# Optimization experiments

Measured on AMD Instinct MI355X. Metric: run time of the kernel, lower is better.

Reference implementation:

```python
import jax, jax.numpy as jnp
import numpy as np

D_MODEL = 768
N_HEADS = 12
D_K = D_MODEL // N_HEADS
LORA_RANK = 8
LORA_ALPHA = 16
SCALING = LORA_ALPHA / LORA_RANK  # lora scaling = alpha / rank
SCALE = float(np.sqrt(D_K))      # attention scale = sqrt(d_k)


def setup_inputs() -> dict:
    key = jax.random.key(0)
    ks = jax.random.split(key, 16)
    s = 0.02
    inp = {
        "x": jax.random.normal(ks[0], (1, 4096, D_MODEL), dtype=jnp.float32),
        # base projections: torch Linear weights are [out, in]
        "wq": jax.random.normal(ks[1], (D_MODEL, D_MODEL), dtype=jnp.float32) * s,
        "bq": jax.random.normal(ks[2], (D_MODEL,), dtype=jnp.float32) * s,
        "wk": jax.random.normal(ks[3], (D_MODEL, D_MODEL), dtype=jnp.float32) * s,
        "bk": jax.random.normal(ks[4], (D_MODEL,), dtype=jnp.float32) * s,
        "wv": jax.random.normal(ks[5], (D_MODEL, D_MODEL), dtype=jnp.float32) * s,
        "bv": jax.random.normal(ks[6], (D_MODEL,), dtype=jnp.float32) * s,
        "wo": jax.random.normal(ks[7], (D_MODEL, D_MODEL), dtype=jnp.float32) * s,
        "bo": jax.random.normal(ks[8], (D_MODEL,), dtype=jnp.float32) * s,
        # LoRA adapters (no bias): down [rank, d_model], up [d_model, rank]
        "wq_down": jax.random.normal(ks[9], (LORA_RANK, D_MODEL), dtype=jnp.float32) * s,
        "wq_up": jax.random.normal(ks[10], (D_MODEL, LORA_RANK), dtype=jnp.float32) * s,
        "wk_down": jax.random.normal(ks[11], (LORA_RANK, D_MODEL), dtype=jnp.float32) * s,
        "wk_up": jax.random.normal(ks[12], (D_MODEL, LORA_RANK), dtype=jnp.float32) * s,
        "wv_down": jax.random.normal(ks[13], (LORA_RANK, D_MODEL), dtype=jnp.float32) * s,
        "wv_up": jax.random.normal(ks[14], (D_MODEL, LORA_RANK), dtype=jnp.float32) * s,
    }
    return inp


def _lora_proj(x, w, b, w_down, w_up):
    # base Linear + scaled LoRA path (dropout = identity at inference)
    base = jnp.einsum("bsd,ed->bse", x, w) + b
    lora = jnp.einsum("bsr,er->bse", jnp.einsum("bsd,rd->bsr", x, w_down), w_up)
    return base + lora * SCALING


def reference(x, wq, bq, wk, bk, wv, bv, wo, bo,
              wq_down, wq_up, wk_down, wk_up, wv_down, wv_up):
    b, s, _ = x.shape
    q = _lora_proj(x, wq, bq, wq_down, wq_up)
    k = _lora_proj(x, wk, bk, wk_down, wk_up)
    v = _lora_proj(x, wv, bv, wv_down, wv_up)
    # [b, h, s, d_k]
    q = q.reshape(b, s, N_HEADS, D_K).transpose(0, 2, 1, 3)
    k = k.reshape(b, s, N_HEADS, D_K).transpose(0, 2, 1, 3)
    v = v.reshape(b, s, N_HEADS, D_K).transpose(0, 2, 1, 3)
    scores = jnp.einsum("bhqd,bhkd->bhqk", q, k) / SCALE
    probs = jax.nn.softmax(scores, axis=-1)
    attn = jnp.einsum("bhqk,bhkd->bhqd", probs, v)
    attn = attn.transpose(0, 2, 1, 3).reshape(b, s, D_MODEL)
    return jnp.einsum("bsd,ed->bse", attn, wo) + bo
```

## Files before the change

### kernel.cpp

```cpp
#include <hip/hip_runtime.h>

typedef unsigned short u16;
typedef __attribute__((ext_vector_type(8))) short short8;
typedef __attribute__((ext_vector_type(4))) float f32x4;
typedef __attribute__((ext_vector_type(16))) float f32x16;
typedef __attribute__((ext_vector_type(4))) unsigned short u16x4;
typedef __attribute__((ext_vector_type(2))) unsigned int uint2v;

typedef __attribute__((address_space(1))) void as1_void;
typedef __attribute__((address_space(3))) void as3_void;

__device__ __forceinline__ void gld16(const u16* g, u16* l) {
  __builtin_amdgcn_global_load_lds((as1_void*)g, (as3_void*)l, 16, 0, 0);
}

__device__ __forceinline__ u16 f2bf(float f) {
  unsigned u = __float_as_uint(f);
  u += 0x7fffu + ((u >> 16) & 1u);
  return (u16)(u >> 16);
}

__device__ __forceinline__ short8 mk8(unsigned a, unsigned b, unsigned c, unsigned d) {
  union { unsigned u[4]; short8 s; } x;
  x.u[0] = a; x.u[1] = b; x.u[2] = c; x.u[3] = d;
  return x.s;
}

__global__ void prep_all(const float* __restrict__ x, u16* __restrict__ xb,
                         const float* __restrict__ wq, const float* __restrict__ wk, const float* __restrict__ wv,
                         const float* __restrict__ dq, const float* __restrict__ uq,
                         const float* __restrict__ dk, const float* __restrict__ uk,
                         const float* __restrict__ dv, const float* __restrict__ uv,
                         const float* __restrict__ wo, u16* __restrict__ weff, u16* __restrict__ wob) {
  int bid = blockIdx.x;
  if (bid < 3072) {
    int i = bid * 256 + threadIdx.x;
    f32x4 f = *(const f32x4*)(x + (size_t)i * 4);
    u16x4 o;
#pragma unroll
    for (int r = 0; r < 4; ++r) o[r] = f2bf(f[r]);
    *(u16x4*)(xb + (size_t)i * 4) = o;
    return;
  }
  if (bid < 4800) {
    int idx = (bid - 3072) * 256 + threadIdx.x;
    int n = idx / 192, d4 = (idx - n * 192) * 4;
    const float *w, *dn, *up; int e;
    if (n < 768)       { w = wq; dn = dq; up = uq; e = n; }
    else if (n < 1536) { w = wk; dn = dk; up = uk; e = n - 768; }
    else               { w = wv; dn = dv; up = uv; e = n - 1536; }
    f32x4 acc = *(const f32x4*)(w + (size_t)e * 768 + d4);
    f32x4 lo = {0.f, 0.f, 0.f, 0.f};
#pragma unroll
    for (int r = 0; r < 8; ++r) {
      float u = up[e * 8 + r];
      f32x4 dv4 = *(const f32x4*)(dn + r * 768 + d4);
#pragma unroll
      for (int j = 0; j < 4; ++j) lo[j] += u * dv4[j];
    }
    u16x4 o;
#pragma unroll
    for (int j = 0; j < 4; ++j) o[j] = f2bf(acc[j] + 2.0f * lo[j]);
    *(u16x4*)(weff + (size_t)n * 768 + d4) = o;
    return;
  }
  int idx = (bid - 4800) * 256 + threadIdx.x;
  f32x4 f = *(const f32x4*)(wo + (size_t)idx * 4);
  u16x4 o;
#pragma unroll
  for (int r = 0; r < 4; ++r) o[r] = f2bf(f[r]);
  *(u16x4*)(wob + (size_t)idx * 4) = o;
}

template <int MT>
__global__ __launch_bounds__(256) void gemm_nt(
    const u16* __restrict__ A, const u16* __restrict__ B, int K, int mode,
    const float* __restrict__ bq, const float* __restrict__ bk, const float* __restrict__ bv,
    u16* __restrict__ qo, u16* __restrict__ ko, u16* __restrict__ vto,
    const float* __restrict__ bo, float* __restrict__ fo) {
  constexpr int NT = (MT == 128) ? 96 : 128;
  constexpr int TI = (MT == 128) ? 4 : 2;
  constexpr int TJ = (MT == 128) ? 3 : 2;
  __shared__ u16 As[2][MT * 32];
  __shared__ u16 Bs[2][NT * 32];
  const int tid = threadIdx.x;
  const int lane = tid & 63;
  const int wid = tid >> 6;
  const int qd = lane >> 4;
  const int m16 = lane & 15;
  const int rowbase = (MT == 128) ? (wid >> 1) * 64 : 0;
  const int colbase = (MT == 128) ? (wid & 1) * 48 : wid * 32;
  const int m0 = blockIdx.x * MT, n0 = blockIdx.y * NT;

  f32x4 acc[TI][TJ];
#pragma unroll
  for (int i = 0; i < TI; ++i)
#pragma unroll
    for (int j = 0; j < TJ; ++j)
#pragma unroll
      for (int e = 0; e < 4; ++e) acc[i][j][e] = 0.f;

  auto stage = [&](int buf, int k0) {
#pragma unroll
    for (int p = tid; p < MT * 4; p += 256) {
      int row = p >> 2;
      int g = (p & 3) ^ ((row >> 1) & 3);
      gld16(A + (size_t)(m0 + row) * K + k0 + g * 8, &As[buf][(p - lane) * 8]);
    }
#pragma unroll
    for (int p = tid; p < NT * 4; p += 256) {
      int row = p >> 2;
      int g = (p & 3) ^ ((row >> 1) & 3);
      gld16(B + (size_t)(n0 + row) * K + k0 + g * 8, &Bs[buf][(p - lane) * 8]);
    }
  };

  stage(0, 0);
  int cur = 0;
  for (int k0 = 0; k0 < K; k0 += 32) {
    __syncthreads();
    if (k0 + 32 < K) stage(cur ^ 1, k0 + 32);
    const u16* as = As[cur];
    const u16* bs = Bs[cur];
    short8 af[TI], bf[TJ];
#pragma unroll
    for (int i = 0; i < TI; ++i) {
      int ar = rowbase + i * 16 + m16;
      af[i] = *(const short8*)&as[(ar * 4 + (qd ^ ((ar >> 1) & 3))) * 8];
    }
#pragma unroll
    for (int j = 0; j < TJ; ++j) {
      int br = colbase + j * 16 + m16;
      bf[j] = *(const short8*)&bs[(br * 4 + (qd ^ ((br >> 1) & 3))) * 8];
    }
#pragma unroll
    for (int i = 0; i < TI; ++i)
#pragma unroll
      for (int j = 0; j < TJ; ++j)
        acc[i][j] = __builtin_amdgcn_mfma_f32_16x16x32_bf16(af[i], bf[j], acc[i][j], 0, 0, 0);
    cur ^= 1;
  }

#pragma unroll
  for (int i = 0; i < TI; ++i) {
    int gr = m0 + rowbase + i * 16 + qd * 4;
#pragma unroll
    for (int j = 0; j < TJ; ++j) {
      int gc = n0 + colbase + j * 16 + m16;
      if (mode == 0) {
        if (gc < 768) {
          float bias = bq[gc];
          int h = gc >> 6, d = gc & 63;
#pragma unroll
          for (int r = 0; r < 4; ++r)
            qo[((size_t)h * 4096 + gr + r) * 64 + d] = f2bf((acc[i][j][r] + bias) * 0.18033688f);
        } else if (gc < 1536) {
          int c = gc - 768;
          float bias = bk[c];
          int h = c >> 6, d = c & 63;
#pragma unroll
          for (int r = 0; r < 4; ++r)
            ko[((size_t)h * 4096 + gr + r) * 64 + d] = f2bf(acc[i][j][r] + bias);
        } else {
          int c = gc - 1536;
          float bias = bv[c];
          int h = c >> 6, d = c & 63;
          u16x4 pk;
#pragma unroll
          for (int r = 0; r < 4; ++r) pk[r] = f2bf(acc[i][j][r] + bias);
          *(u16x4*)&vto[((size_t)h * 64 + d) * 4096 + gr] = pk;
        }
      } else {
        float bias = bo[gc];
#pragma unroll
        for (int r = 0; r < 4; ++r)
          fo[(size_t)(gr + r) * 768 + gc] = acc[i][j][r] + bias;
      }
    }
  }
}

__global__ __launch_bounds__(512, 4) void attn_fwd(
    const u16* __restrict__ Q, const u16* __restrict__ Kg, const u16* __restrict__ Vt,
    float* __restrict__ Opart, float* __restrict__ lpart, u16* __restrict__ abo, int kspl) {
  __shared__ u16 Ks[2][64 * 64];
  __shared__ u16 Vs[2][64 * 64];
  const int tid = threadIdx.x, lane = tid & 63, wid = tid >> 6;
  const int q32 = lane & 31, hf = lane >> 5;
  const int grp = blockIdx.x;
  const int h = grp / kspl;
  const int z = grp - h * kspl;
  const int qrow = blockIdx.y * 256 + wid * 32;
  const int kbase = z * (4096 / kspl);
  const int niter = (4096 / kspl) >> 6;

  const u16* kgh = Kg + (size_t)h * 4096 * 64;
  const u16* vth = Vt + (size_t)h * 64 * 4096;

  short8 qf[4];
  {
    const u16* qb = Q + ((size_t)h * 4096 + qrow + q32) * 64 + hf * 8;
#pragma unroll
    for (int ds = 0; ds < 4; ++ds) qf[ds] = *(const short8*)(qb + ds * 16);
  }

  float lrun = 0.f;
  f32x16 oacc[2];
#pragma unroll
  for (int d = 0; d < 2; ++d)
#pragma unroll
    for (int r = 0; r < 16; ++r) oacc[d][r] = 0.f;

  f32x16 zv;
#pragma unroll
  for (int r = 0; r < 16; ++r) zv[r] = 0.f;

  {
    const int kt = kbase;
    int p = tid;
    int row = p >> 3;
    int g = (p & 7) ^ (row & 7);
    gld16(kgh + (size_t)(kt + row) * 64 + g * 8, &Ks[0][(p - lane) * 8]);
    gld16(vth + (size_t)row * 4096 + kt + g * 8, &Vs[0][(p - lane) * 8]);
  }

  for (int it = 0; it < niter; ++it) {
    __syncthreads();
    if (it + 1 < niter) {
      const int kt = kbase + (it + 1) * 64;
      const int b = (it + 1) & 1;
      int p = tid;
      int row = p >> 3;
      int g = (p & 7) ^ (row & 7);
      gld16(kgh + (size_t)(kt + row) * 64 + g * 8, &Ks[b][(p - lane) * 8]);
      gld16(vth + (size_t)row * 4096 + kt + g * 8, &Vs[b][(p - lane) * 8]);
    }
    const u16* ks = Ks[it & 1];
    const u16* vs = Vs[it & 1];

#pragma unroll
    for (int kst = 0; kst < 2; ++kst) {
      const int krow = kst * 32 + q32;
      short8 kf[4];
#pragma unroll
      for (int ds = 0; ds < 4; ++ds) {
        int c = ds * 2 + hf;
        kf[ds] = *(const short8*)&ks[((krow << 3) + (c ^ (krow & 7))) * 8];
      }
      f32x16 s;
      __builtin_amdgcn_s_setprio(1);
      s = __builtin_amdgcn_mfma_f32_32x32x16_bf16(kf[0], qf[0], zv, 0, 0, 0);
#pragma unroll
      for (int ds = 1; ds < 4; ++ds)
        s = __builtin_amdgcn_mfma_f32_32x32x16_bf16(kf[ds], qf[ds], s, 0, 0, 0);
      __builtin_amdgcn_s_setprio(0);
      unsigned w[8];
      float ls0 = 0.f, ls1 = 0.f;
#pragma unroll
      for (int i = 0; i < 8; ++i) {
        float p0 = __builtin_amdgcn_exp2f(s[2 * i]);
        float p1 = __builtin_amdgcn_exp2f(s[2 * i + 1]);
        if (i & 1) ls1 += p0 + p1; else ls0 += p0 + p1;
        asm("v_cvt_pk_bf16_f32 %0, %1, %2" : "=v"(w[i]) : "v"(p0), "v"(p1));
      }
      lrun += ls0 + ls1;
      uint2v r0 = __builtin_amdgcn_permlane32_swap(w[0], w[2], false, false);
      uint2v r1 = __builtin_amdgcn_permlane32_swap(w[1], w[3], false, false);
      uint2v r2 = __builtin_amdgcn_permlane32_swap(w[4], w[6], false, false);
      uint2v r3 = __builtin_amdgcn_permlane32_swap(w[5], w[7], false, false);
      short8 pa[2];
      pa[0] = mk8(r0[0], r1[0], r0[1], r1[1]);
      pa[1] = mk8(r2[0], r3[0], r2[1], r3[1]);
      __builtin_amdgcn_s_setprio(1);
#pragma unroll
      for (int dt = 0; dt < 2; ++dt) {
        const int vrow = dt * 32 + q32;
#pragma unroll
        for (int ksl = 0; ksl < 2; ++ksl) {
          int c = kst * 4 + ksl * 2 + hf;
          short8 vf = *(const short8*)&vs[((vrow << 3) + (c ^ (vrow & 7))) * 8];
          oacc[dt] = __builtin_amdgcn_mfma_f32_32x32x16_bf16(pa[ksl], vf, oacc[dt], 0, 0, 0);
        }
      }
      __builtin_amdgcn_s_setprio(0);
    }
  }

  lrun += __shfl_xor(lrun, 32);

  if (kspl > 1) {
    if (hf == 0)
      lpart[((size_t)z * 4096 + qrow + q32) * 12 + h] = lrun;
    float* ob = Opart + (size_t)z * 4096 * 768;
#pragma unroll
    for (int r = 0; r < 16; ++r) {
      int qloc = (r & 3) + 8 * (r >> 2) + 4 * hf;
#pragma unroll
      for (int dt = 0; dt < 2; ++dt)
        ob[(size_t)(qrow + qloc) * 768 + h * 64 + dt * 32 + q32] = oacc[dt][r];
    }
  } else {
    float linv = 1.0f / lrun;
#pragma unroll
    for (int r = 0; r < 16; ++r) {
      int qloc = (r & 3) + 8 * (r >> 2) + 4 * hf;
      float li = __shfl(linv, qloc);
#pragma unroll
      for (int dt = 0; dt < 2; ++dt)
        abo[(size_t)(qrow + qloc) * 768 + h * 64 + dt * 32 + q32] =
            f2bf(oacc[dt][r] * li);
    }
  }
}

__global__ void merge_norm(const float* __restrict__ Opart, const float* __restrict__ lpart,
                           u16* __restrict__ abo, int ksp) {
  int i = blockIdx.x * 256 + threadIdx.x;
  int s = i / 192, cq = i - s * 192;
  int h = cq >> 4;
  f32x4 a = {0.f, 0.f, 0.f, 0.f};
  float l = 0.f;
  for (int z = 0; z < ksp; ++z) {
    f32x4 b = *(const f32x4*)(Opart + (size_t)z * 4096 * 768 + (size_t)i * 4);
#pragma unroll
    for (int r = 0; r < 4; ++r) a[r] += b[r];
    l += lpart[((size_t)z * 4096 + s) * 12 + h];
  }
  float rl = 1.0f / l;
  u16x4 o;
#pragma unroll
  for (int r = 0; r < 4; ++r) o[r] = f2bf(a[r] * rl);
  *(u16x4*)(abo + (size_t)i * 4) = o;
}

extern "C" void kernel_launch(void* const* d_in, const int* in_sizes, int n_in,
                              void* d_out, int out_size, void* d_ws, size_t ws_size,
                              hipStream_t stream) {
  const float* x   = (const float*)d_in[0];
  const float* wq  = (const float*)d_in[1];
  const float* bq  = (const float*)d_in[2];
  const float* wk  = (const float*)d_in[3];
  const float* bk  = (const float*)d_in[4];
  const float* wv  = (const float*)d_in[5];
  const float* bv  = (const float*)d_in[6];
  const float* wo  = (const float*)d_in[7];
  const float* bo  = (const float*)d_in[8];
  const float* dq  = (const float*)d_in[9];
  const float* uq  = (const float*)d_in[10];
  const float* dk  = (const float*)d_in[11];
  const float* uk  = (const float*)d_in[12];
  const float* dv  = (const float*)d_in[13];
  const float* uv  = (const float*)d_in[14];
  float* out = (float*)d_out;

  char* ws = (char*)d_ws;
  u16* xb    = (u16*)(ws);
  u16* ab    = (u16*)(ws);
  u16* weff  = (u16*)(ws + 6291456);
  u16* wob   = (u16*)(ws + 9830400);
  u16* qb    = (u16*)(ws + 11010048);
  u16* kb    = (u16*)(ws + 17301504);
  u16* vtb   = (u16*)(ws + 23592960);
  float* Op  = (float*)(ws + 29884416);
  float* lp  = (float*)(ws + 80216064);

  int kspl = 1;
  if (ws_size >= 81002496ull) kspl = 4;
  else if (ws_size >= 55443456ull) {
    kspl = 2;
    lp = (float*)(ws + 55050240);
  }

  prep_all<<<5376, 256, 0, stream>>>(x, xb, wq, wk, wv, dq, uq, dk, uk, dv, uv, wo, weff, wob);
  gemm_nt<128><<<dim3(32, 24), 256, 0, stream>>>(xb, weff, 768, 0, bq, bk, bv, qb, kb, vtb,
                                                 nullptr, nullptr);
  attn_fwd<<<dim3(12 * kspl, 16), 512, 0, stream>>>(qb, kb, vtb, Op, lp, ab, kspl);
  if (kspl > 1) merge_norm<<<3072, 256, 0, stream>>>(Op, lp, ab, kspl);
  gemm_nt<32><<<dim3(128, 6), 256, 0, stream>>>(ab, wob, 768, 1, nullptr, nullptr, nullptr,
                                                nullptr, nullptr, nullptr, bo, out);
}
```

Before: 207.7 us.

## Fuse split-K attention merge and normalization into output projection GEMM A-load

Removes the separate merge_norm kernel. The output-projection GEMM now reads the fp32 partial attention outputs directly, sums the split partitions, normalizes them with per-row inverse sums precomputed into LDS, converts to bf16 and writes the A tile into shared memory. This saves one launch and the bf16 round trip through global memory. In exchange, A staging moves from async DMA to register loads that overlap the MFMA loop, and the fp32 partials get re-read by all 6 column blocks.

```diff
diff --git a/kernel.cpp b/kernel.cpp
--- a/kernel.cpp
+++ b/kernel.cpp
@@ -77,12 +77,14 @@
     const u16* __restrict__ A, const u16* __restrict__ B, int K, int mode,
     const float* __restrict__ bq, const float* __restrict__ bk, const float* __restrict__ bv,
     u16* __restrict__ qo, u16* __restrict__ ko, u16* __restrict__ vto,
-    const float* __restrict__ bo, float* __restrict__ fo) {
+    const float* __restrict__ bo, float* __restrict__ fo,
+    const float* __restrict__ OpA, const float* __restrict__ lpA, int ksp) {
   constexpr int NT = (MT == 128) ? 96 : 128;
   constexpr int TI = (MT == 128) ? 4 : 2;
   constexpr int TJ = (MT == 128) ? 3 : 2;
   __shared__ u16 As[2][MT * 32];
   __shared__ u16 Bs[2][NT * 32];
+  __shared__ float linv_lds[12][32];
   const int tid = threadIdx.x;
   const int lane = tid & 63;
   const int wid = tid >> 6;
@@ -91,6 +93,7 @@
   const int rowbase = (MT == 128) ? (wid >> 1) * 64 : 0;
   const int colbase = (MT == 128) ? (wid & 1) * 48 : wid * 32;
   const int m0 = blockIdx.x * MT, n0 = blockIdx.y * NT;
+  const bool fused = (mode == 1) && (ksp > 1);
 
   f32x4 acc[TI][TJ];
 #pragma unroll
@@ -100,26 +103,68 @@
 #pragma unroll
       for (int e = 0; e < 4; ++e) acc[i][j][e] = 0.f;
 
-  auto stage = [&](int buf, int k0) {
+  const int fc = tid >> 1, fhh = tid & 1;
+  const int frow = fc >> 2;
+  const int fg = (fc & 3) ^ ((frow >> 1) & 3);
+  const int feo = fg * 8 + fhh * 4;
+  f32x4 aregs[4];
+
+  auto stageB = [&](int buf, int k0) {
+#pragma unroll
+    for (int p = tid; p < NT * 4; p += 256) {
+      int row = p >> 2;
+      int g = (p & 3) ^ ((row >> 1) & 3);
+      gld16(B + (size_t)(n0 + row) * K + k0 + g * 8, &Bs[buf][(p - lane) * 8]);
+    }
+  };
+  auto stageA_dma = [&](int buf, int k0) {
 #pragma unroll
     for (int p = tid; p < MT * 4; p += 256) {
       int row = p >> 2;
       int g = (p & 3) ^ ((row >> 1) & 3);
       gld16(A + (size_t)(m0 + row) * K + k0 + g * 8, &As[buf][(p - lane) * 8]);
     }
-#pragma unroll
-    for (int p = tid; p < NT * 4; p += 256) {
-      int row = p >> 2;
-      int g = (p & 3) ^ ((row >> 1) & 3);
-      gld16(B + (size_t)(n0 + row) * K + k0 + g * 8, &Bs[buf][(p - lane) * 8]);
-    }
   };
-
-  stage(0, 0);
+  auto loadA = [&](int k0) {
+    const float* src = OpA + (size_t)(m0 + frow) * 768 + k0 + feo;
+    for (int z = 0; z < ksp; ++z)
+      aregs[z] = *(const f32x4*)(src + (size_t)z * 4096 * 768);
+  };
+  auto writeA = [&](int buf, int k0) {
+    float li = linv_lds[k0 >> 6][frow];
+    f32x4 a = aregs[0];
+    for (int z = 1; z < ksp; ++z)
+#pragma unroll
+      for (int r = 0; r < 4; ++r) a[r] += aregs[z][r];
+    u16x4 o;
+#pragma unroll
+    for (int r = 0; r < 4; ++r) o[r] = f2bf(a[r] * li);
+    *(u16x4*)&As[buf][fc * 8 + fhh * 4] = o;
+  };
+
+  if (fused) {
+    for (int t = tid; t < 384; t += 256) {
+      int hh = t >> 5, sl = t & 31;
+      float l = 0.f;
+      for (int z = 0; z < ksp; ++z) l += lpA[((size_t)z * 4096 + m0 + sl) * 12 + hh];
+      linv_lds[hh][sl] = 1.0f / l;
+    }
+    __syncthreads();
+    loadA(0);
+    stageB(0, 0);
+    writeA(0, 0);
+  } else {
+    stageA_dma(0, 0);
+    stageB(0, 0);
+  }
+
   int cur = 0;
   for (int k0 = 0; k0 < K; k0 += 32) {
     __syncthreads();
-    if (k0 + 32 < K) stage(cur ^ 1, k0 + 32);
+    if (k0 + 32 < K) {
+      if (fused) { loadA(k0 + 32); stageB(cur ^ 1, k0 + 32); }
+      else       { stageA_dma(cur ^ 1, k0 + 32); stageB(cur ^ 1, k0 + 32); }
+    }
     const u16* as = As[cur];
     const u16* bs = Bs[cur];
     short8 af[TI], bf[TJ];
@@ -138,6 +183,7 @@
 #pragma unroll
       for (int j = 0; j < TJ; ++j)
         acc[i][j] = __builtin_amdgcn_mfma_f32_16x16x32_bf16(af[i], bf[j], acc[i][j], 0, 0, 0);
+    if (fused && k0 + 32 < K) writeA(cur ^ 1, k0 + 32);
     cur ^= 1;
   }
 
@@ -311,26 +357,6 @@
             f2bf(oacc[dt][r] * li);
     }
   }
-}
-
-__global__ void merge_norm(const float* __restrict__ Opart, const float* __restrict__ lpart,
-                           u16* __restrict__ abo, int ksp) {
-  int i = blockIdx.x * 256 + threadIdx.x;
-  int s = i / 192, cq = i - s * 192;
-  int h = cq >> 4;
-  f32x4 a = {0.f, 0.f, 0.f, 0.f};
-  float l = 0.f;
-  for (int z = 0; z < ksp; ++z) {
-    f32x4 b = *(const f32x4*)(Opart + (size_t)z * 4096 * 768 + (size_t)i * 4);
-#pragma unroll
-    for (int r = 0; r < 4; ++r) a[r] += b[r];
-    l += lpart[((size_t)z * 4096 + s) * 12 + h];
-  }
-  float rl = 1.0f / l;
-  u16x4 o;
-#pragma unroll
-  for (int r = 0; r < 4; ++r) o[r] = f2bf(a[r] * rl);
-  *(u16x4*)(abo + (size_t)i * 4) = o;
 }
 
 extern "C" void kernel_launch(void* const* d_in, const int* in_sizes, int n_in,
@@ -373,9 +399,8 @@
 
   prep_all<<<5376, 256, 0, stream>>>(x, xb, wq, wk, wv, dq, uq, dk, uk, dv, uv, wo, weff, wob);
   gemm_nt<128><<<dim3(32, 24), 256, 0, stream>>>(xb, weff, 768, 0, bq, bk, bv, qb, kb, vtb,
-                                                 nullptr, nullptr);
+                                                 nullptr, nullptr, nullptr, nullptr, 1);
   attn_fwd<<<dim3(12 * kspl, 16), 512, 0, stream>>>(qb, kb, vtb, Op, lp, ab, kspl);
-  if (kspl > 1) merge_norm<<<3072, 256, 0, stream>>>(Op, lp, ab, kspl);
   gemm_nt<32><<<dim3(128, 6), 256, 0, stream>>>(ab, wob, 768, 1, nullptr, nullptr, nullptr,
-                                                nullptr, nullptr, nullptr, bo, out);
-}
+                                                nullptr, nullptr, nullptr, bo, out, Op, lp, kspl);
+}
```

After: 236.3 us. +13.8%, slower.
